# Kernel optimization log

Hardware: AMD Instinct MI355X
Metric: run time of the kernel (lower is better)

## Reference

```python
import jax, jax.numpy as jnp
import numpy as np
import math

IMG_SIZE = 768
NUM_CLASSES = 90
THRESHOLD = 0.05
IOU_THRESHOLD = 0.5
MAX_DETECTIONS = 100
K_CAND = 512  # per-class candidate pool before greedy NMS
RATIOS = [(1.0, 1.0), (1.4, 0.7), (0.7, 1.4)]
SCALES = [2 ** 0, 2 ** (1.0 / 3.0), 2 ** (2.0 / 3.0)]


def _generate_anchors():
    anchor_scale = 4.0
    pyramid_levels = [3, 4, 5, 6, 7]
    all_levels = []
    for lv in pyramid_levels:
        stride = 2 ** lv
        size = anchor_scale * 2 ** lv
        grid = IMG_SIZE // stride
        sx = np.arange(grid) * stride
        sy, sx = np.meshgrid(np.arange(grid) * stride, sx, indexing='ij')
        # torch meshgrid(shift_y, shift_x, indexing='ij') -> rows are y
        yy, xx = np.meshgrid(np.arange(grid) * stride, np.arange(grid) * stride, indexing='ij')
        shifts = np.stack([xx.ravel(), yy.ravel(), xx.ravel(), yy.ravel()], axis=1).astype(np.float32)
        base = []
        for r in RATIOS:
            for s in SCALES:
                w = size * s * math.sqrt(r[0] / r[1])
                h = size * s * math.sqrt(r[1] / r[0])
                base.append([-w / 2, -h / 2, w / 2, h / 2])
        base = np.asarray(base, dtype=np.float32)  # [9,4]
        anc = (base[None, :, :] + shifts[:, None, :]).reshape(-1, 4)
        all_levels.append(anc)
    return np.concatenate(all_levels, axis=0)  # [110484,4]


def setup_inputs() -> dict:
    key = jax.random.key(0)
    k1, k2, k3 = jax.random.split(key, 3)
    A = 110484
    x = jax.random.normal(k1, (1, 3, IMG_SIZE, IMG_SIZE), dtype=jnp.float32)
    regression = jax.random.normal(k2, (1, A, 4), dtype=jnp.float32) * 0.3
    classification = jax.random.normal(k3, (1, A, NUM_CLASSES), dtype=jnp.float32) - 2.0
    anchors = jnp.asarray(_generate_anchors())
    return {"x": x, "regression": regression, "classification": classification, "anchors": anchors}


def _decode_and_clip(anchors, deltas, H, W):
    # BBoxTransform (RetinaNet-style): deltas = (dx, dy, dw, dh)
    wa = anchors[:, 2] - anchors[:, 0]
    ha = anchors[:, 3] - anchors[:, 1]
    cxa = anchors[:, 0] + 0.5 * wa
    cya = anchors[:, 1] + 0.5 * ha
    dx, dy, dw, dh = deltas[:, 0], deltas[:, 1], deltas[:, 2], deltas[:, 3]
    cx = cxa + dx * wa
    cy = cya + dy * ha
    w = jnp.exp(dw) * wa
    h = jnp.exp(dh) * ha
    x1 = jnp.clip(cx - 0.5 * w, 0.0, W)
    y1 = jnp.clip(cy - 0.5 * h, 0.0, H)
    x2 = jnp.clip(cx + 0.5 * w, 0.0, W)
    y2 = jnp.clip(cy + 0.5 * h, 0.0, H)
    return jnp.stack([x1, y1, x2, y2], axis=1)  # [A,4]


def _pairwise_iou(b):  # [K,4] -> [K,K]
    area = (b[:, 2] - b[:, 0]) * (b[:, 3] - b[:, 1])
    xx1 = jnp.maximum(b[:, None, 0], b[None, :, 0])
    yy1 = jnp.maximum(b[:, None, 1], b[None, :, 1])
    xx2 = jnp.minimum(b[:, None, 2], b[None, :, 2])
    yy2 = jnp.minimum(b[:, None, 3], b[None, :, 3])
    inter = jnp.clip(xx2 - xx1, 0.0) * jnp.clip(yy2 - yy1, 0.0)
    return inter / (area[:, None] + area[None, :] - inter + 1e-8)


def _greedy_nms(iou_c, valid_c):
    # boxes are pre-sorted by descending score; fixed-iteration greedy NMS
    def step(suppressed, i):
        keep_i = valid_c[i] & jnp.logical_not(suppressed[i])
        suppressed = jnp.where(keep_i, suppressed | (iou_c[i] > IOU_THRESHOLD), suppressed)
        return suppressed, keep_i
    _, keep = jax.lax.scan(step, jnp.zeros(iou_c.shape[0], dtype=bool), jnp.arange(iou_c.shape[0]))
    return keep  # [K]


def _postprocess(x, regression, classification, anchors):
    H, W = x.shape[2], x.shape[3]
    boxes = _decode_and_clip(anchors, regression[0], float(H), float(W))  # [A,4]
    scores = jax.nn.sigmoid(classification[0])                            # [A,C]
    # per-class top-K candidate pool (sorted desc), fixed-shape NMS
    vals, idx = jax.lax.top_k(scores.T, K_CAND)        # [C,K]
    cand = boxes[idx]                                   # [C,K,4]
    valid = vals > THRESHOLD                            # [C,K]
    iou = jax.vmap(_pairwise_iou)(cand)                 # [C,K,K]
    keep = jax.vmap(_greedy_nms)(iou, valid)            # [C,K]
    kept_scores = jnp.where(keep, vals, -1.0).reshape(-1)  # [C*K]
    top_vals, flat_idx = jax.lax.top_k(kept_scores, MAX_DETECTIONS)
    labels = (flat_idx // K_CAND).astype(jnp.float32)
    det_boxes = cand.reshape(-1, 4)[flat_idx]
    ok = top_vals > 0.0
    det = jnp.concatenate([
        jnp.zeros((MAX_DETECTIONS, 1), dtype=jnp.float32),  # batch ids (batch=1 -> 0)
        det_boxes,
        top_vals[:, None],
        labels[:, None],
    ], axis=1)  # [100,7]
    return jnp.where(ok[:, None], det, 0.0)


def reference(x, regression, classification, anchors):
    return _postprocess(x, regression, classification, anchors)
```

## Files before the change

kernel.cpp:

```cpp
#include <hip/hip_runtime.h>
#include <math.h>


#define A_N   110484
#define C_N   90
#define KCAND 512
#define NBINS 8192
#define KSH   19
#define MAXDET 100
#define IMG_F 768.0f
#define THRESH 0.05f
#define VTOT  (A_N / 4)
#define SL_CAP 2048
#define KEEP_CAP 100
#define T_BLKS ((A_N + 63) / 64)
#define PD_BLKS ((A_N + 255) / 256)
#define SEL_T 1024
#define FCAP  512

typedef unsigned int u32;
typedef unsigned long long u64;

__device__ __forceinline__ u32 fkey(float f) {
    u32 u = __float_as_uint(f);
    return (u & 0x80000000u) ? ~u : (u | 0x80000000u);
}
__device__ __forceinline__ float unfkey(u32 k) {
    u32 u = (k & 0x80000000u) ? (k ^ 0x80000000u) : ~k;
    return __uint_as_float(u);
}
__device__ __forceinline__ u64 shflx64(u64 v, int m) {
    u32 lo = (u32)__shfl_xor((int)(u32)v, m, 64);
    u32 hi = (u32)__shfl_xor((int)(v >> 32), m, 64);
    return ((u64)hi << 32) | lo;
}

__global__ __launch_bounds__(256)
void prep_kernel(const float* __restrict__ cls,
                 const float* __restrict__ anchors,
                 const float* __restrict__ reg,
                 u32* __restrict__ keysT,
                 float4* __restrict__ boxes) {
    __shared__ u32 tile[64 * 91];
    if (blockIdx.x >= T_BLKS) {
        int a = (blockIdx.x - T_BLKS) * 256 + threadIdx.x;
        if (a < A_N) {
            float4 an = ((const float4*)anchors)[a];
            float4 dl = ((const float4*)reg)[a];
            float wa = an.z - an.x, ha = an.w - an.y;
            float cx = an.x + 0.5f * wa + dl.x * wa;
            float cy = an.y + 0.5f * ha + dl.y * ha;
            float w = expf(dl.z) * wa;
            float h = expf(dl.w) * ha;
            float4 o;
            o.x = fminf(fmaxf(cx - 0.5f * w, 0.0f), IMG_F);
            o.y = fminf(fmaxf(cy - 0.5f * h, 0.0f), IMG_F);
            o.z = fminf(fmaxf(cx + 0.5f * w, 0.0f), IMG_F);
            o.w = fminf(fmaxf(cy + 0.5f * h, 0.0f), IMG_F);
            boxes[a] = o;
        }
        return;
    }
    const int a0 = blockIdx.x * 64;
    const int lim = min(64, A_N - a0);
    const int n4 = (lim * C_N) >> 2;
    const float4* src4 = (const float4*)(cls + (size_t)a0 * C_N);
    for (int i4 = threadIdx.x; i4 < n4; i4 += 256) {
        float4 x4 = src4[i4];
        const u32 base = (u32)(4 * i4);
        float xs[4] = { x4.x, x4.y, x4.z, x4.w };
        #pragma unroll
        for (int k = 0; k < 4; ++k) {
            u32 i = base + k;
            u32 aa = i / C_N, c = i % C_N;
            float s = 1.0f / (1.0f + expf(-xs[k]));
            tile[aa * 91 + c] = fkey(s);
        }
    }
    __syncthreads();
    for (int j = threadIdx.x; j < C_N * 64; j += 256) {
        int c = j >> 6, aa = j & 63;
        if (aa < lim)
            keysT[(size_t)c * A_N + a0 + aa] = tile[aa * 91 + c];
    }
}

__global__ __launch_bounds__(SEL_T, 4)
void selnms_kernel(const u32* __restrict__ keysT,
                   const float4* __restrict__ boxes,
                   u32* __restrict__ keptbuf, u32* __restrict__ cnt2) {
    __shared__ __align__(16) u32 smem[11264];
    u32* hist = smem;
    u32* csum = smem + 4096;
    u64* lbuf = (u64*)(smem + 5120);
    float4* bb4 = (float4*)smem;
    float* sc = (float*)(smem + 2048);
    u32* keepf = smem + 2560;
    u32* wbase = smem + 2576;
    u32* bmask = smem + 2608;
    __shared__ u32 sPv;
    __shared__ int lcnt;
    const int tid = threadIdx.x;
    const int c = blockIdx.x;
    const int l = tid & 63, w = tid >> 6;
    const uint4* kv = (const uint4*)(keysT + (size_t)c * A_N);

    for (int i = tid; i < NBINS / 2; i += SEL_T) hist[i] = 0;
    if (tid == 0) { sPv = 0; lcnt = 0; }
    __syncthreads();

    #define HACC(K) do { \
        u32 b0 = (K).x >> KSH, b1 = (K).y >> KSH, b2 = (K).z >> KSH, b3 = (K).w >> KSH; \
        atomicAdd(&hist[b0 >> 1], 1u << ((b0 & 1) << 4)); \
        atomicAdd(&hist[b1 >> 1], 1u << ((b1 & 1) << 4)); \
        atomicAdd(&hist[b2 >> 1], 1u << ((b2 & 1) << 4)); \
        atomicAdd(&hist[b3 >> 1], 1u << ((b3 & 1) << 4)); } while (0)
    {
        int i = tid;
        for (; i + 7 * SEL_T < VTOT; i += 8 * SEL_T) {
            uint4 k0 = kv[i], k1 = kv[i + SEL_T], k2 = kv[i + 2 * SEL_T], k3 = kv[i + 3 * SEL_T];
            uint4 k4 = kv[i + 4 * SEL_T], k5 = kv[i + 5 * SEL_T], k6 = kv[i + 6 * SEL_T], k7 = kv[i + 7 * SEL_T];
            HACC(k0); HACC(k1); HACC(k2); HACC(k3);
            HACC(k4); HACC(k5); HACC(k6); HACC(k7);
        }
        for (; i < VTOT; i += SEL_T) { uint4 ka = kv[i]; HACC(ka); }
    }
    __syncthreads();

    u32 own = 0;
    {
        const int wb = (NBINS / 2) - 4 - 4 * tid;
        const int g = (tid >> 3) & 3;
        #pragma unroll
        for (int jj = 0; jj < 4; ++jj) {
            u32 v = hist[wb + ((g + jj) & 3)];
            own += (v & 0xffffu) + (v >> 16);
        }
    }
    csum[tid] = own;
    __syncthreads();
    for (int off = 1; off < SEL_T; off <<= 1) {
        u32 v = csum[tid];
        u32 a = (tid >= off) ? csum[tid - off] : 0u;
        __syncthreads();
        csum[tid] = v + a;
        __syncthreads();
    }
    const u32 incl = csum[tid], excl = incl - own;
    if (excl < (u32)KCAND && incl >= (u32)KCAND) {
        u32 cum = excl;
        const int hb = NBINS - 1 - 8 * tid;
        for (int j = 0; j < 8; ++j) {
            int b = hb - j;
            u32 v = hist[b >> 1];
            u32 cnt = (b & 1) ? (v >> 16) : (v & 0xffffu);
            if (cum + cnt >= (u32)KCAND) { sPv = (u32)b; break; }
            cum += cnt;
        }
    }
    __syncthreads();
    const u32 P = sPv;

    #define CACC(K, BASE) do { \
        if (((K).x >> KSH) >= P) { int p = atomicAdd(&lcnt, 1); if (p < SL_CAP) lbuf[p] = (((u64)(~(K).x)) << 32) | (u32)(BASE); } \
        if (((K).y >> KSH) >= P) { int p = atomicAdd(&lcnt, 1); if (p < SL_CAP) lbuf[p] = (((u64)(~(K).y)) << 32) | (u32)((BASE) + 1); } \
        if (((K).z >> KSH) >= P) { int p = atomicAdd(&lcnt, 1); if (p < SL_CAP) lbuf[p] = (((u64)(~(K).z)) << 32) | (u32)((BASE) + 2); } \
        if (((K).w >> KSH) >= P) { int p = atomicAdd(&lcnt, 1); if (p < SL_CAP) lbuf[p] = (((u64)(~(K).w)) << 32) | (u32)((BASE) + 3); } } while (0)
    {
        int i = tid;
        for (; i + 7 * SEL_T < VTOT; i += 8 * SEL_T) {
            uint4 k0 = kv[i], k1 = kv[i + SEL_T], k2 = kv[i + 2 * SEL_T], k3 = kv[i + 3 * SEL_T];
            uint4 k4 = kv[i + 4 * SEL_T], k5 = kv[i + 5 * SEL_T], k6 = kv[i + 6 * SEL_T], k7 = kv[i + 7 * SEL_T];
            CACC(k0, 4 * i); CACC(k1, 4 * (i + SEL_T)); CACC(k2, 4 * (i + 2 * SEL_T)); CACC(k3, 4 * (i + 3 * SEL_T));
            CACC(k4, 4 * (i + 4 * SEL_T)); CACC(k5, 4 * (i + 5 * SEL_T)); CACC(k6, 4 * (i + 6 * SEL_T)); CACC(k7, 4 * (i + 7 * SEL_T));
        }
        for (; i < VTOT; i += SEL_T) { uint4 ka = kv[i]; CACC(ka, 4 * i); }
    }
    __syncthreads();
    const int n = min(lcnt, SL_CAP);
    for (int q = tid; q < SL_CAP; q += SEL_T) if (q >= n) lbuf[q] = ~0ULL;
    __syncthreads();

    const int i0 = 128 * w + l, i1 = i0 + 64;
    u64 v0, v1;
    {
        v0 = lbuf[i0]; v1 = lbuf[i1];
        __syncthreads();
        #pragma unroll
        for (u32 kk = 2; kk <= (u32)SL_CAP; kk <<= 1) {
            #pragma unroll
            for (u32 j = kk >> 1; j > 0; j >>= 1) {
                if (j >= 128) {
                    lbuf[i0] = v0; lbuf[i1] = v1;
                    __syncthreads();
                    u64 w0 = lbuf[i0 ^ j], w1 = lbuf[i1 ^ j];
                    bool m0 = (((i0 & j) == 0) == ((i0 & kk) == 0));
                    bool m1 = (((i1 & j) == 0) == ((i1 & kk) == 0));
                    v0 = m0 ? (v0 < w0 ? v0 : w0) : (v0 > w0 ? v0 : w0);
                    v1 = m1 ? (v1 < w1 ? v1 : w1) : (v1 > w1 ? v1 : w1);
                    __syncthreads();
                } else if (j == 64) {
                    bool up = ((i0 & kk) == 0);
                    u64 mn = v0 < v1 ? v0 : v1, mx = v0 < v1 ? v1 : v0;
                    v0 = up ? mn : mx; v1 = up ? mx : mn;
                } else {
                    u64 w0 = shflx64(v0, (int)j), w1 = shflx64(v1, (int)j);
                    bool m0 = (((i0 & j) == 0) == ((i0 & kk) == 0));
                    bool m1 = (((i1 & j) == 0) == ((i1 & kk) == 0));
                    v0 = m0 ? (v0 < w0 ? v0 : w0) : (v0 > w0 ? v0 : w0);
                    v1 = m1 ? (v1 < w1 ? v1 : w1) : (v1 > w1 ? v1 : w1);
                }
            }
        }
    }
    __syncthreads();

    if (w < 4) {
        sc[i0] = unfkey(~((u32)(v0 >> 32)));
        sc[i1] = unfkey(~((u32)(v1 >> 32)));
        bb4[i0] = boxes[(u32)v0];
        bb4[i1] = boxes[(u32)v1];
    }
    if (tid < 16) keepf[tid] = 0;
    __syncthreads();

    {
        const float4 cj0 = bb4[0 * 64 + l], cj1 = bb4[1 * 64 + l];
        const float4 cj2 = bb4[2 * 64 + l], cj3 = bb4[3 * 64 + l];
        const float4 cj4 = bb4[4 * 64 + l], cj5 = bb4[5 * 64 + l];
        const float4 cj6 = bb4[6 * 64 + l], cj7 = bb4[7 * 64 + l];
        const float aj0 = (cj0.z - cj0.x) * (cj0.w - cj0.y);
        const float aj1 = (cj1.z - cj1.x) * (cj1.w - cj1.y);
        const float aj2 = (cj2.z - cj2.x) * (cj2.w - cj2.y);
        const float aj3 = (cj3.z - cj3.x) * (cj3.w - cj3.y);
        const float aj4 = (cj4.z - cj4.x) * (cj4.w - cj4.y);
        const float aj5 = (cj5.z - cj5.x) * (cj5.w - cj5.y);
        const float aj6 = (cj6.z - cj6.x) * (cj6.w - cj6.y);
        const float aj7 = (cj7.z - cj7.x) * (cj7.w - cj7.y);

        #define QSTEP(QQ, CJ, AJ) do { \
            if (QQ >= q0) { \
                float xx1 = fmaxf(bi.x, (CJ).x), yy1 = fmaxf(bi.y, (CJ).y); \
                float xx2 = fminf(bi.z, (CJ).z), yy2 = fminf(bi.w, (CJ).w); \
                float inter = fmaxf(xx2 - xx1, 0.0f) * fmaxf(yy2 - yy1, 0.0f); \
                float uni = ai + (AJ) - inter + 1e-8f; \
                bool sup = ((QQ * 64 + l) > r) && (inter > 0.5f * uni); \
                u64 bal = __ballot(sup); \
                if (l == 0) *(u64*)(row + 2 * QQ) = bal; \
            } } while (0)

        for (int r = w; r < KCAND; r += 16) {
            const float4 bi = bb4[r];
            const float ai = (bi.z - bi.x) * (bi.w - bi.y);
            const int q0 = (r + 1) >> 6;
            u32* row = bmask + r * 16;
            if (l < 2 * q0) row[l] = 0;
            QSTEP(0, cj0, aj0); QSTEP(1, cj1, aj1);
            QSTEP(2, cj2, aj2); QSTEP(3, cj3, aj3);
            QSTEP(4, cj4, aj4); QSTEP(5, cj5, aj5);
            QSTEP(6, cj6, aj6); QSTEP(7, cj7, aj7);
        }
        #undef QSTEP
    }
    __syncthreads();

    if (tid < 64) {
        const int lw = tid & 15;
        u32 removed = 0, keepw = 0;
        u32 rA[8], rB[8]; float sA[8], sB[8];
        #pragma unroll
        for (int k = 0; k < 8; ++k) { rA[k] = bmask[k * 16 + lw]; sA[k] = sc[k]; }
        #pragma unroll 1
        for (int ch = 0; ch < 64; ch += 2) {
            const int tb1 = (ch + 1) * 8;
            #pragma unroll
            for (int k = 0; k < 8; ++k) { rB[k] = bmask[(tb1 + k) * 16 + lw]; sB[k] = sc[tb1 + k]; }
            {
                const int tb = ch * 8;
                #pragma unroll
                for (int k = 0; k < 8; ++k) {
                    const int t = tb + k;
                    u32 rw = (u32)__builtin_amdgcn_readlane((int)removed, t >> 5);
                    bool d = (sA[k] > THRESH) && (((rw >> (t & 31)) & 1u) == 0u);
                    removed |= d ? rA[k] : 0u;
                    keepw |= (d && (tid == (t >> 5))) ? (1u << (t & 31)) : 0u;
                }
            }
            const int tb2 = (ch + 2 < 64) ? (ch + 2) * 8 : 0;
            #pragma unroll
            for (int k = 0; k < 8; ++k) { rA[k] = bmask[(tb2 + k) * 16 + lw]; sA[k] = sc[tb2 + k]; }
            {
                #pragma unroll
                for (int k = 0; k < 8; ++k) {
                    const int t = tb1 + k;
                    u32 rw = (u32)__builtin_amdgcn_readlane((int)removed, t >> 5);
                    bool d = (sB[k] > THRESH) && (((rw >> (t & 31)) & 1u) == 0u);
                    removed |= d ? rB[k] : 0u;
                    keepw |= (d && (tid == (t >> 5))) ? (1u << (t & 31)) : 0u;
                }
            }
            u32 cnt = (u32)__popc(keepw);
            #pragma unroll
            for (int m = 32; m; m >>= 1) cnt += (u32)__shfl_xor((int)cnt, m, 64);
            if (cnt >= (u32)KEEP_CAP) break;
        }
        if (tid < 16) keepf[tid] = keepw;
    }
    __syncthreads();

    if (tid == 0) {
        u32 t = 0;
        for (int q = 0; q < 16; ++q) { wbase[q] = t; t += __popc(keepf[q]); }
        wbase[16] = t;
        cnt2[c] = (t < (u32)KEEP_CAP) ? t : (u32)KEEP_CAP;
    }
    __syncthreads();
    if (tid < KCAND) {
        u32 word = keepf[tid >> 5];
        u32 bit = (u32)tid & 31u;
        if ((word >> bit) & 1u) {
            u32 rank = wbase[tid >> 5] + __popc(word & ((1u << bit) - 1u));
            if (rank < (u32)KEEP_CAP) {
                float s = sc[tid];
                float4 b = bb4[tid];
                uint4 a2, b2;
                a2.x = ~fkey(s);
                a2.y = (u32)(c * KCAND + tid);
                a2.z = __float_as_uint(b.x);
                a2.w = __float_as_uint(b.y);
                b2.x = __float_as_uint(b.z);
                b2.y = __float_as_uint(b.w);
                b2.z = __float_as_uint(s);
                b2.w = 0u;
                uint4* e = (uint4*)(keptbuf + ((size_t)c * KEEP_CAP + rank) * 8);
                e[0] = a2; e[1] = b2;
            }
        }
    }
}

__global__ __launch_bounds__(1024)
void final_kernel(const u32* __restrict__ keptbuf, const u32* __restrict__ cnt2,
                  float* __restrict__ out) {
    __shared__ u32 hist[NBINS];
    __shared__ u32 csum[1024];
    __shared__ u64 ebuf[FCAP];
    __shared__ u32 eidx[FCAP];
    __shared__ u32 scnt[C_N];
    __shared__ u32 sP;
    __shared__ int sN;
    const int tid = threadIdx.x;
    const int TOT = C_N * KEEP_CAP;

    for (int i = tid; i < MAXDET * 7; i += 1024) out[i] = 0.0f;
    for (int i = tid; i < NBINS; i += 1024) hist[i] = 0;
    if (tid < C_N) scnt[tid] = cnt2[tid];
    if (tid == 0) { sN = 0; sP = NBINS - 1; }
    __syncthreads();

    for (int i = tid; i < TOT; i += 1024) {
        u32 c = (u32)i / KEEP_CAP, pp = (u32)i % KEEP_CAP;
        if (pp < scnt[c]) {
            u32 khi = keptbuf[(size_t)i * 8];
            atomicAdd(&hist[khi >> KSH], 1u);
        }
    }
    __syncthreads();
    u32 own = 0; const int lo = 8 * tid;
    #pragma unroll
    for (int j = 0; j < 8; ++j) own += hist[lo + j];
    csum[tid] = own;
    __syncthreads();
    for (int off = 1; off < 1024; off <<= 1) {
        u32 v = csum[tid];
        u32 a = (tid >= off) ? csum[tid - off] : 0u;
        __syncthreads();
        csum[tid] = v + a;
        __syncthreads();
    }
    const u32 incl = csum[tid], excl = incl - own;
    if (excl < (u32)MAXDET && incl >= (u32)MAXDET) {
        u32 cum = excl;
        for (int j = 0; j < 8; ++j) {
            u32 h = hist[lo + j];
            if (cum + h >= (u32)MAXDET) { sP = (u32)(lo + j); break; }
            cum += h;
        }
    }
    __syncthreads();
    const u32 P = sP;
    for (int i = tid; i < TOT; i += 1024) {
        u32 c = (u32)i / KEEP_CAP, pp = (u32)i % KEEP_CAP;
        if (pp < scnt[c]) {
            const uint2 v2 = *((const uint2*)(keptbuf + (size_t)i * 8));
            if ((v2.x >> KSH) <= P) {
                int p = atomicAdd(&sN, 1);
                if (p < FCAP) {
                    ebuf[p] = ((u64)v2.x << 32) | v2.y;
                    eidx[p] = (u32)i;
                }
            }
        }
    }
    __syncthreads();
    const int n = min(sN, FCAP);
    u32 m = 128; while ((int)m < n) m <<= 1;
    for (int i = tid; i < (int)m; i += 1024) if (i >= n) ebuf[i] = ~0ULL;
    __syncthreads();
    for (u32 kk = 2; kk <= m; kk <<= 1) {
        for (u32 j = kk >> 1; j > 0; j >>= 1) {
            u32 i = (u32)tid;
            if (i < m) {
                u32 ixj = i ^ j;
                if (ixj > i) {
                    u64 x = ebuf[i], y = ebuf[ixj];
                    bool up = ((i & kk) == 0);
                    if (up ? (x > y) : (x < y)) {
                        ebuf[i] = y; ebuf[ixj] = x;
                        u32 t = eidx[i]; eidx[i] = eidx[ixj]; eidx[ixj] = t;
                    }
                }
            }
            __syncthreads();
        }
    }
    if (tid < MAXDET && tid < n) {
        u64 comp = ebuf[tid];
        if (comp != ~0ULL) {
            const uint4* e = (const uint4*)(keptbuf + (size_t)eidx[tid] * 8);
            uint4 a = e[0], b = e[1];
            float* o = out + tid * 7;
            o[0] = 0.0f;
            o[1] = __uint_as_float(a.z); o[2] = __uint_as_float(a.w);
            o[3] = __uint_as_float(b.x); o[4] = __uint_as_float(b.y);
            o[5] = __uint_as_float(b.z);
            o[6] = (float)(((u32)comp) >> 9);
        }
    }
}

extern "C" void kernel_launch(void* const* d_in, const int* in_sizes, int n_in,
                              void* d_out, int out_size, void* d_ws, size_t ws_size,
                              hipStream_t stream) {
    const float* reg     = (const float*)d_in[1];
    const float* cls     = (const float*)d_in[2];
    const float* anchors = (const float*)d_in[3];
    float* out = (float*)d_out;

    char* ws = (char*)d_ws;
    size_t off = 0;
    auto alloc = [&](size_t bytes) -> void* {
        void* p = ws + off;
        off = (off + bytes + 255) & ~(size_t)255;
        return p;
    };
    u32*    keysT   = (u32*)   alloc((size_t)C_N * A_N * sizeof(u32));
    float4* boxes   = (float4*)alloc((size_t)A_N * sizeof(float4));
    u32*    keptbuf = (u32*)   alloc((size_t)C_N * KEEP_CAP * 8 * sizeof(u32));
    u32*    cnt2    = (u32*)   alloc((size_t)C_N * sizeof(u32));
    (void)ws_size;

    prep_kernel<<<T_BLKS + PD_BLKS, 256, 0, stream>>>(cls, anchors, reg, keysT, boxes);
    selnms_kernel<<<C_N, SEL_T, 0, stream>>>(keysT, boxes, keptbuf, cnt2);
    final_kernel<<<1, 1024, 0, stream>>>(keptbuf, cnt2, out);
}
```

Baseline: 188.2 us.

## Store 16-bit logit keys transposed and recompute exact sigmoid only for candidates

The prep kernel now writes the top 16 bits of the order-preserving logit key instead of the full 32-bit sigmoid key. This halves the transposed key buffer written and then read twice by the selection kernel. The selection kernel builds the histogram and picks the threshold on these truncated keys. It collects only candidate indices, then re-reads the original logits to compute exact sigmoid scores for the sort. It also swaps the block-wide shared-memory prefix scan for a wave-shuffle scan and restructures the IoU mask loop to keep fewer boxes in registers. The risk is that keys tied in the top 16 bits can push more entries past the candidate buffer capacity, and the gathered logit reads are strided.

```diff
diff --git a/kernel.cpp b/kernel.cpp
--- a/kernel.cpp
+++ b/kernel.cpp
@@ -10,7 +10,8 @@
 #define MAXDET 100
 #define IMG_F 768.0f
 #define THRESH 0.05f
-#define VTOT  (A_N / 4)
+#define ROW16 (A_N + 4)
+#define VT8   (ROW16 / 8)
 #define SL_CAP 2048
 #define KEEP_CAP 100
 #define T_BLKS ((A_N + 63) / 64)
@@ -19,6 +20,7 @@
 #define FCAP  512
 
 typedef unsigned int u32;
+typedef unsigned short u16;
 typedef unsigned long long u64;
 
 __device__ __forceinline__ u32 fkey(float f) {
@@ -39,10 +41,14 @@
 void prep_kernel(const float* __restrict__ cls,
                  const float* __restrict__ anchors,
                  const float* __restrict__ reg,
-                 u32* __restrict__ keysT,
+                 u16* __restrict__ keysT16,
                  float4* __restrict__ boxes) {
     __shared__ u32 tile[64 * 91];
     if (blockIdx.x >= T_BLKS) {
+        if (blockIdx.x == T_BLKS && threadIdx.x < C_N * 4) {
+            int c = threadIdx.x >> 2, off = threadIdx.x & 3;
+            keysT16[(size_t)c * ROW16 + A_N + off] = 0;
+        }
         int a = (blockIdx.x - T_BLKS) * 256 + threadIdx.x;
         if (a < A_N) {
             float4 an = ((const float4*)anchors)[a];
@@ -73,57 +79,66 @@
         for (int k = 0; k < 4; ++k) {
             u32 i = base + k;
             u32 aa = i / C_N, c = i % C_N;
-            float s = 1.0f / (1.0f + expf(-xs[k]));
-            tile[aa * 91 + c] = fkey(s);
-        }
-    }
-    __syncthreads();
-    for (int j = threadIdx.x; j < C_N * 64; j += 256) {
-        int c = j >> 6, aa = j & 63;
-        if (aa < lim)
-            keysT[(size_t)c * A_N + a0 + aa] = tile[aa * 91 + c];
+            tile[aa * 91 + c] = fkey(xs[k]) >> 16;
+        }
+    }
+    __syncthreads();
+    for (int j = threadIdx.x; j < C_N * 32; j += 256) {
+        int c = j >> 5, pr = j & 31;
+        int aa0 = 2 * pr;
+        if (aa0 < lim) {
+            u32 v = tile[aa0 * 91 + c] | (tile[(aa0 + 1) * 91 + c] << 16);
+            *((u32*)(keysT16 + (size_t)c * ROW16 + a0) + pr) = v;
+        }
     }
 }
 
 __global__ __launch_bounds__(SEL_T, 4)
-void selnms_kernel(const u32* __restrict__ keysT,
+void selnms_kernel(const u16* __restrict__ keysT16,
+                   const float* __restrict__ cls,
                    const float4* __restrict__ boxes,
                    u32* __restrict__ keptbuf, u32* __restrict__ cnt2) {
-    __shared__ __align__(16) u32 smem[11264];
-    u32* hist = smem;
-    u32* csum = smem + 4096;
-    u64* lbuf = (u64*)(smem + 5120);
+    __shared__ __align__(16) u32 smem[10800];
+    u32* hist  = smem;
+    u32* idx32 = smem + 4096;
+    u64* cand64 = (u64*)smem;
     float4* bb4 = (float4*)smem;
-    float* sc = (float*)(smem + 2048);
+    float* sc  = (float*)(smem + 2048);
     u32* keepf = smem + 2560;
     u32* wbase = smem + 2576;
     u32* bmask = smem + 2608;
+    __shared__ u32 wsum[16];
     __shared__ u32 sPv;
     __shared__ int lcnt;
     const int tid = threadIdx.x;
     const int c = blockIdx.x;
     const int l = tid & 63, w = tid >> 6;
-    const uint4* kv = (const uint4*)(keysT + (size_t)c * A_N);
+    const uint4* kv = (const uint4*)(keysT16 + (size_t)c * ROW16);
 
     for (int i = tid; i < NBINS / 2; i += SEL_T) hist[i] = 0;
     if (tid == 0) { sPv = 0; lcnt = 0; }
     __syncthreads();
 
-    #define HACC(K) do { \
-        u32 b0 = (K).x >> KSH, b1 = (K).y >> KSH, b2 = (K).z >> KSH, b3 = (K).w >> KSH; \
-        atomicAdd(&hist[b0 >> 1], 1u << ((b0 & 1) << 4)); \
-        atomicAdd(&hist[b1 >> 1], 1u << ((b1 & 1) << 4)); \
-        atomicAdd(&hist[b2 >> 1], 1u << ((b2 & 1) << 4)); \
-        atomicAdd(&hist[b3 >> 1], 1u << ((b3 & 1) << 4)); } while (0)
+    #define HONE(B) atomicAdd(&hist[(B) >> 1], 1u << (((B) & 1) << 4))
+    #define HACC8(K) do { \
+        u32 w0 = (K).x, w1 = (K).y, w2 = (K).z, w3 = (K).w; \
+        HONE((w0 & 0xffffu) >> 3); HONE(w0 >> 19); \
+        HONE((w1 & 0xffffu) >> 3); HONE(w1 >> 19); \
+        HONE((w2 & 0xffffu) >> 3); HONE(w2 >> 19); \
+        HONE((w3 & 0xffffu) >> 3); HONE(w3 >> 19); } while (0)
     {
         int i = tid;
-        for (; i + 7 * SEL_T < VTOT; i += 8 * SEL_T) {
+        for (; i + 7 * SEL_T < VT8; i += 8 * SEL_T) {
             uint4 k0 = kv[i], k1 = kv[i + SEL_T], k2 = kv[i + 2 * SEL_T], k3 = kv[i + 3 * SEL_T];
             uint4 k4 = kv[i + 4 * SEL_T], k5 = kv[i + 5 * SEL_T], k6 = kv[i + 6 * SEL_T], k7 = kv[i + 7 * SEL_T];
-            HACC(k0); HACC(k1); HACC(k2); HACC(k3);
-            HACC(k4); HACC(k5); HACC(k6); HACC(k7);
-        }
-        for (; i < VTOT; i += SEL_T) { uint4 ka = kv[i]; HACC(ka); }
+            HACC8(k0); HACC8(k1); HACC8(k2); HACC8(k3);
+            HACC8(k4); HACC8(k5); HACC8(k6); HACC8(k7);
+        }
+        for (; i + 3 * SEL_T < VT8; i += 4 * SEL_T) {
+            uint4 k0 = kv[i], k1 = kv[i + SEL_T], k2 = kv[i + 2 * SEL_T], k3 = kv[i + 3 * SEL_T];
+            HACC8(k0); HACC8(k1); HACC8(k2); HACC8(k3);
+        }
+        for (; i < VT8; i += SEL_T) { uint4 ka = kv[i]; HACC8(ka); }
     }
     __syncthreads();
 
@@ -137,79 +152,98 @@
             own += (v & 0xffffu) + (v >> 16);
         }
     }
-    csum[tid] = own;
-    __syncthreads();
-    for (int off = 1; off < SEL_T; off <<= 1) {
-        u32 v = csum[tid];
-        u32 a = (tid >= off) ? csum[tid - off] : 0u;
+    {
+        u32 x = own;
+        #pragma unroll
+        for (int off = 1; off < 64; off <<= 1) {
+            u32 y = (u32)__shfl_up((int)x, off, 64);
+            if (l >= off) x += y;
+        }
+        if (l == 63) wsum[w] = x;
         __syncthreads();
-        csum[tid] = v + a;
-        __syncthreads();
-    }
-    const u32 incl = csum[tid], excl = incl - own;
-    if (excl < (u32)KCAND && incl >= (u32)KCAND) {
-        u32 cum = excl;
-        const int hb = NBINS - 1 - 8 * tid;
-        for (int j = 0; j < 8; ++j) {
-            int b = hb - j;
-            u32 v = hist[b >> 1];
-            u32 cnt = (b & 1) ? (v >> 16) : (v & 0xffffu);
-            if (cum + cnt >= (u32)KCAND) { sPv = (u32)b; break; }
-            cum += cnt;
-        }
-    }
-    __syncthreads();
-    const u32 P = sPv;
-
-    #define CACC(K, BASE) do { \
-        if (((K).x >> KSH) >= P) { int p = atomicAdd(&lcnt, 1); if (p < SL_CAP) lbuf[p] = (((u64)(~(K).x)) << 32) | (u32)(BASE); } \
-        if (((K).y >> KSH) >= P) { int p = atomicAdd(&lcnt, 1); if (p < SL_CAP) lbuf[p] = (((u64)(~(K).y)) << 32) | (u32)((BASE) + 1); } \
-        if (((K).z >> KSH) >= P) { int p = atomicAdd(&lcnt, 1); if (p < SL_CAP) lbuf[p] = (((u64)(~(K).z)) << 32) | (u32)((BASE) + 2); } \
-        if (((K).w >> KSH) >= P) { int p = atomicAdd(&lcnt, 1); if (p < SL_CAP) lbuf[p] = (((u64)(~(K).w)) << 32) | (u32)((BASE) + 3); } } while (0)
+        u32 wpre = 0;
+        for (int ww = 0; ww < w; ++ww) wpre += wsum[ww];
+        const u32 incl = wpre + x, excl = incl - own;
+        if (excl < (u32)KCAND && incl >= (u32)KCAND) {
+            u32 cum = excl;
+            const int hb = NBINS - 1 - 8 * tid;
+            for (int j = 0; j < 8; ++j) {
+                int b = hb - j;
+                u32 v = hist[b >> 1];
+                u32 cnt = (b & 1) ? (v >> 16) : (v & 0xffffu);
+                if (cum + cnt >= (u32)KCAND) { sPv = (u32)b; break; }
+                cum += cnt;
+            }
+        }
+    }
+    __syncthreads();
+    const u32 P3 = sPv << 3;
+
+    #define CONE(KK, AA) do { \
+        if ((KK) >= P3) { int p = atomicAdd(&lcnt, 1); if (p < SL_CAP) idx32[p] = (u32)(AA); } } while (0)
+    #define CACC8(K, BASE) do { \
+        u32 w0 = (K).x, w1 = (K).y, w2 = (K).z, w3 = (K).w; \
+        CONE(w0 & 0xffffu, (BASE));     CONE(w0 >> 16, (BASE) + 1); \
+        CONE(w1 & 0xffffu, (BASE) + 2); CONE(w1 >> 16, (BASE) + 3); \
+        CONE(w2 & 0xffffu, (BASE) + 4); CONE(w2 >> 16, (BASE) + 5); \
+        CONE(w3 & 0xffffu, (BASE) + 6); CONE(w3 >> 16, (BASE) + 7); } while (0)
     {
         int i = tid;
-        for (; i + 7 * SEL_T < VTOT; i += 8 * SEL_T) {
+        for (; i + 7 * SEL_T < VT8; i += 8 * SEL_T) {
             uint4 k0 = kv[i], k1 = kv[i + SEL_T], k2 = kv[i + 2 * SEL_T], k3 = kv[i + 3 * SEL_T];
             uint4 k4 = kv[i + 4 * SEL_T], k5 = kv[i + 5 * SEL_T], k6 = kv[i + 6 * SEL_T], k7 = kv[i + 7 * SEL_T];
-            CACC(k0, 4 * i); CACC(k1, 4 * (i + SEL_T)); CACC(k2, 4 * (i + 2 * SEL_T)); CACC(k3, 4 * (i + 3 * SEL_T));
-            CACC(k4, 4 * (i + 4 * SEL_T)); CACC(k5, 4 * (i + 5 * SEL_T)); CACC(k6, 4 * (i + 6 * SEL_T)); CACC(k7, 4 * (i + 7 * SEL_T));
-        }
-        for (; i < VTOT; i += SEL_T) { uint4 ka = kv[i]; CACC(ka, 4 * i); }
+            CACC8(k0, 8 * i); CACC8(k1, 8 * (i + SEL_T)); CACC8(k2, 8 * (i + 2 * SEL_T)); CACC8(k3, 8 * (i + 3 * SEL_T));
+            CACC8(k4, 8 * (i + 4 * SEL_T)); CACC8(k5, 8 * (i + 5 * SEL_T)); CACC8(k6, 8 * (i + 6 * SEL_T)); CACC8(k7, 8 * (i + 7 * SEL_T));
+        }
+        for (; i + 3 * SEL_T < VT8; i += 4 * SEL_T) {
+            uint4 k0 = kv[i], k1 = kv[i + SEL_T], k2 = kv[i + 2 * SEL_T], k3 = kv[i + 3 * SEL_T];
+            CACC8(k0, 8 * i); CACC8(k1, 8 * (i + SEL_T)); CACC8(k2, 8 * (i + 2 * SEL_T)); CACC8(k3, 8 * (i + 3 * SEL_T));
+        }
+        for (; i < VT8; i += SEL_T) { uint4 ka = kv[i]; CACC8(ka, 8 * i); }
     }
     __syncthreads();
     const int n = min(lcnt, SL_CAP);
-    for (int q = tid; q < SL_CAP; q += SEL_T) if (q >= n) lbuf[q] = ~0ULL;
+
+    for (int q = tid; q < SL_CAP; q += SEL_T) {
+        u64 comp = ~0ULL;
+        if (q < n) {
+            u32 a = idx32[q];
+            if (a < A_N) {
+                float lg = cls[(size_t)a * C_N + c];
+                float s = 1.0f / (1.0f + expf(-lg));
+                comp = ((u64)(~fkey(s)) << 32) | a;
+            }
+        }
+        cand64[q] = comp;
+    }
     __syncthreads();
 
     const int i0 = 128 * w + l, i1 = i0 + 64;
-    u64 v0, v1;
-    {
-        v0 = lbuf[i0]; v1 = lbuf[i1];
-        __syncthreads();
+    u64 v0 = cand64[i0], v1 = cand64[i1];
+    __syncthreads();
+    #pragma unroll
+    for (u32 kk = 2; kk <= (u32)SL_CAP; kk <<= 1) {
         #pragma unroll
-        for (u32 kk = 2; kk <= (u32)SL_CAP; kk <<= 1) {
-            #pragma unroll
-            for (u32 j = kk >> 1; j > 0; j >>= 1) {
-                if (j >= 128) {
-                    lbuf[i0] = v0; lbuf[i1] = v1;
-                    __syncthreads();
-                    u64 w0 = lbuf[i0 ^ j], w1 = lbuf[i1 ^ j];
-                    bool m0 = (((i0 & j) == 0) == ((i0 & kk) == 0));
-                    bool m1 = (((i1 & j) == 0) == ((i1 & kk) == 0));
-                    v0 = m0 ? (v0 < w0 ? v0 : w0) : (v0 > w0 ? v0 : w0);
-                    v1 = m1 ? (v1 < w1 ? v1 : w1) : (v1 > w1 ? v1 : w1);
-                    __syncthreads();
-                } else if (j == 64) {
-                    bool up = ((i0 & kk) == 0);
-                    u64 mn = v0 < v1 ? v0 : v1, mx = v0 < v1 ? v1 : v0;
-                    v0 = up ? mn : mx; v1 = up ? mx : mn;
-                } else {
-                    u64 w0 = shflx64(v0, (int)j), w1 = shflx64(v1, (int)j);
-                    bool m0 = (((i0 & j) == 0) == ((i0 & kk) == 0));
-                    bool m1 = (((i1 & j) == 0) == ((i1 & kk) == 0));
-                    v0 = m0 ? (v0 < w0 ? v0 : w0) : (v0 > w0 ? v0 : w0);
-                    v1 = m1 ? (v1 < w1 ? v1 : w1) : (v1 > w1 ? v1 : w1);
-                }
+        for (u32 j = kk >> 1; j > 0; j >>= 1) {
+            if (j >= 128) {
+                cand64[i0] = v0; cand64[i1] = v1;
+                __syncthreads();
+                u64 w0 = cand64[i0 ^ j], w1 = cand64[i1 ^ j];
+                bool m0 = (((i0 & j) == 0) == ((i0 & kk) == 0));
+                bool m1 = (((i1 & j) == 0) == ((i1 & kk) == 0));
+                v0 = m0 ? (v0 < w0 ? v0 : w0) : (v0 > w0 ? v0 : w0);
+                v1 = m1 ? (v1 < w1 ? v1 : w1) : (v1 > w1 ? v1 : w1);
+                __syncthreads();
+            } else if (j == 64) {
+                bool up = ((i0 & kk) == 0);
+                u64 mn = v0 < v1 ? v0 : v1, mx = v0 < v1 ? v1 : v0;
+                v0 = up ? mn : mx; v1 = up ? mx : mn;
+            } else {
+                u64 w0 = shflx64(v0, (int)j), w1 = shflx64(v1, (int)j);
+                bool m0 = (((i0 & j) == 0) == ((i0 & kk) == 0));
+                bool m1 = (((i1 & j) == 0) == ((i1 & kk) == 0));
+                v0 = m0 ? (v0 < w0 ? v0 : w0) : (v0 > w0 ? v0 : w0);
+                v1 = m1 ? (v1 < w1 ? v1 : w1) : (v1 > w1 ? v1 : w1);
             }
         }
     }
@@ -224,43 +258,29 @@
     if (tid < 16) keepf[tid] = 0;
     __syncthreads();
 
-    {
-        const float4 cj0 = bb4[0 * 64 + l], cj1 = bb4[1 * 64 + l];
-        const float4 cj2 = bb4[2 * 64 + l], cj3 = bb4[3 * 64 + l];
-        const float4 cj4 = bb4[4 * 64 + l], cj5 = bb4[5 * 64 + l];
-        const float4 cj6 = bb4[6 * 64 + l], cj7 = bb4[7 * 64 + l];
-        const float aj0 = (cj0.z - cj0.x) * (cj0.w - cj0.y);
-        const float aj1 = (cj1.z - cj1.x) * (cj1.w - cj1.y);
-        const float aj2 = (cj2.z - cj2.x) * (cj2.w - cj2.y);
-        const float aj3 = (cj3.z - cj3.x) * (cj3.w - cj3.y);
-        const float aj4 = (cj4.z - cj4.x) * (cj4.w - cj4.y);
-        const float aj5 = (cj5.z - cj5.x) * (cj5.w - cj5.y);
-        const float aj6 = (cj6.z - cj6.x) * (cj6.w - cj6.y);
-        const float aj7 = (cj7.z - cj7.x) * (cj7.w - cj7.y);
-
-        #define QSTEP(QQ, CJ, AJ) do { \
-            if (QQ >= q0) { \
-                float xx1 = fmaxf(bi.x, (CJ).x), yy1 = fmaxf(bi.y, (CJ).y); \
-                float xx2 = fminf(bi.z, (CJ).z), yy2 = fminf(bi.w, (CJ).w); \
-                float inter = fmaxf(xx2 - xx1, 0.0f) * fmaxf(yy2 - yy1, 0.0f); \
-                float uni = ai + (AJ) - inter + 1e-8f; \
-                bool sup = ((QQ * 64 + l) > r) && (inter > 0.5f * uni); \
-                u64 bal = __ballot(sup); \
-                if (l == 0) *(u64*)(row + 2 * QQ) = bal; \
-            } } while (0)
-
+    for (int r = w; r < KCAND; r += 16) {
+        const int q0 = (r + 1) >> 6;
+        if (l < 2 * q0) bmask[r * 16 + l] = 0;
+    }
+    #pragma unroll 1
+    for (int q = 0; q < 8; ++q) {
+        const int j = q * 64 + l;
+        const float4 cj = bb4[j];
+        const float aj = (cj.z - cj.x) * (cj.w - cj.y);
         for (int r = w; r < KCAND; r += 16) {
-            const float4 bi = bb4[r];
-            const float ai = (bi.z - bi.x) * (bi.w - bi.y);
             const int q0 = (r + 1) >> 6;
-            u32* row = bmask + r * 16;
-            if (l < 2 * q0) row[l] = 0;
-            QSTEP(0, cj0, aj0); QSTEP(1, cj1, aj1);
-            QSTEP(2, cj2, aj2); QSTEP(3, cj3, aj3);
-            QSTEP(4, cj4, aj4); QSTEP(5, cj5, aj5);
-            QSTEP(6, cj6, aj6); QSTEP(7, cj7, aj7);
-        }
-        #undef QSTEP
+            if (q >= q0) {
+                const float4 bi = bb4[r];
+                const float ai = (bi.z - bi.x) * (bi.w - bi.y);
+                float xx1 = fmaxf(bi.x, cj.x), yy1 = fmaxf(bi.y, cj.y);
+                float xx2 = fminf(bi.z, cj.z), yy2 = fminf(bi.w, cj.w);
+                float inter = fmaxf(xx2 - xx1, 0.0f) * fmaxf(yy2 - yy1, 0.0f);
+                float uni = ai + aj - inter + 1e-8f;
+                bool sup = (j > r) && (inter > 0.5f * uni);
+                u64 bal = __ballot(sup);
+                if (l == 0) *(u64*)(bmask + r * 16 + 2 * q) = bal;
+            }
+        }
     }
     __syncthreads();
 
@@ -454,13 +474,13 @@
         off = (off + bytes + 255) & ~(size_t)255;
         return p;
     };
-    u32*    keysT   = (u32*)   alloc((size_t)C_N * A_N * sizeof(u32));
+    u16*    keysT16 = (u16*)   alloc((size_t)C_N * ROW16 * sizeof(u16));
     float4* boxes   = (float4*)alloc((size_t)A_N * sizeof(float4));
     u32*    keptbuf = (u32*)   alloc((size_t)C_N * KEEP_CAP * 8 * sizeof(u32));
     u32*    cnt2    = (u32*)   alloc((size_t)C_N * sizeof(u32));
     (void)ws_size;
 
-    prep_kernel<<<T_BLKS + PD_BLKS, 256, 0, stream>>>(cls, anchors, reg, keysT, boxes);
-    selnms_kernel<<<C_N, SEL_T, 0, stream>>>(keysT, boxes, keptbuf, cnt2);
+    prep_kernel<<<T_BLKS + PD_BLKS, 256, 0, stream>>>(cls, anchors, reg, keysT16, boxes);
+    selnms_kernel<<<C_N, SEL_T, 0, stream>>>(keysT16, cls, boxes, keptbuf, cnt2);
     final_kernel<<<1, 1024, 0, stream>>>(keptbuf, cnt2, out);
 }
```

Measured after the change: 197.6 us. 5.0% more time.
